# Kernel tuning notes

Measured on AMD Instinct MI355X. Metric: run time of the kernel, lower is better.

## Reference

```python
import jax, jax.numpy as jnp
import numpy as np

N, D, E = 32768, 768, 8
F = 4 * D  # 3072


def setup_inputs() -> dict:
    key = jax.random.key(0)
    ks = jax.random.split(key, 8)
    scale = 0.02
    hidden_states = jax.random.normal(ks[0], (N, D), dtype=jnp.float32)
    Wg = jax.random.normal(ks[1], (E, D), dtype=jnp.float32) * scale  # gate, no bias
    W1 = jax.random.normal(ks[2], (E, F, D), dtype=jnp.float32) * scale
    b1 = jnp.zeros((E, F), dtype=jnp.float32)
    W2 = jax.random.normal(ks[3], (E, D, F), dtype=jnp.float32) * scale
    b2 = jnp.zeros((E, D), dtype=jnp.float32)
    W3 = jax.random.normal(ks[4], (E, 1, D), dtype=jnp.float32) * scale
    b3 = jnp.zeros((E, 1), dtype=jnp.float32)
    return {"hidden_states": hidden_states, "Wg": Wg, "W1": W1, "b1": b1,
            "W2": W2, "b2": b2, "W3": W3, "b3": b3, "top_k": 2}


def reference(hidden_states, Wg, W1, b1, W2, b2, W3, b3, top_k):
    x = hidden_states  # [N, D]
    logits = x @ Wg.T  # [N, E]
    probs = jax.nn.softmax(logits.astype(jnp.float32), axis=-1)
    w, _sel = jax.lax.top_k(probs, top_k)  # [N, k] (descending)
    w = (w / w.sum(axis=-1, keepdims=True)).astype(x.dtype)
    # FAITHFUL TO SOURCE BUG: expert used is the position index j (experts[j]),
    # not the selected expert id. So densely run experts 0..top_k-1 on all tokens.
    W1k, b1k = W1[:top_k], b1[:top_k]
    W2k, b2k = W2[:top_k], b2[:top_k]
    W3k, b3k = W3[:top_k], b3[:top_k]
    # dropout is identity in eval mode
    h = jax.nn.relu(jnp.einsum('nd,kfd->knf', x, W1k) + b1k[:, None, :])  # [k,N,F]
    o = x[None, :, :] + jnp.einsum('knf,kdf->knd', h, W2k) + b2k[:, None, :]  # residual, [k,N,D]
    s = jnp.einsum('knd,kod->kno', o, W3k) + b3k[:, None, :]  # [k,N,1]
    out = jnp.sum(jnp.swapaxes(w, 0, 1)[:, :, None] * s, axis=0)  # [N,1]
    return out
```

## Files before the change

kernel.cpp:

```cpp
#include <hip/hip_runtime.h>
#include <hip/hip_bf16.h>
#include <stdint.h>

#define N_TOK 32768
#define DDIM  768
#define FDIM  3072
#define NCOLS (2*FDIM)
#define BK    32
#define KTILES (DDIM/BK)
#define NTILES (NCOLS/128)
#define VD_CHUNK 96

typedef __attribute__((ext_vector_type(8))) short bf16x8;
typedef __attribute__((ext_vector_type(4))) float f32x4;

__device__ __forceinline__ unsigned short f2bf(float f) {
  unsigned u = __builtin_bit_cast(unsigned, f);
  unsigned r = (u + 0x7fffu + ((u >> 16) & 1u)) >> 16;
  return (unsigned short)r;
}

__device__ __forceinline__ void gl_lds16(const void* g, void* l) {
  __builtin_amdgcn_global_load_lds(
      (const __attribute__((address_space(1))) unsigned int*)g,
      (__attribute__((address_space(3))) unsigned int*)l, 16, 0, 0);
}

__global__ __launch_bounds__(256) void cvt_kernel(const float* __restrict__ src,
                                                  unsigned short* __restrict__ dst) {
  size_t i = ((size_t)blockIdx.x * 256 + threadIdx.x) * 4;
  float4 f = *(const float4*)(src + i);
  ushort4 u;
  u.x = f2bf(f.x); u.y = f2bf(f.y); u.z = f2bf(f.z); u.w = f2bf(f.w);
  *(ushort4*)(dst + i) = u;
}

__global__ __launch_bounds__(256) void vcalc_kernel(const float* __restrict__ W2,
                                                    const float* __restrict__ W3,
                                                    float* __restrict__ vpart) {
  __shared__ float w3s[VD_CHUNK];
  int k  = blockIdx.x / 12;
  int fb = blockIdx.x % 12;
  int db = blockIdx.y;
  if (threadIdx.x < VD_CHUNK) w3s[threadIdx.x] = W3[k*DDIM + db*VD_CHUNK + threadIdx.x];
  __syncthreads();
  int f = fb*256 + threadIdx.x;
  const float* W2k = W2 + (size_t)k*DDIM*FDIM + (size_t)db*VD_CHUNK*FDIM + f;
  float s = 0.f;
  #pragma unroll 8
  for (int d = 0; d < VD_CHUNK; ++d) s += W2k[(size_t)d*FDIM] * w3s[d];
  vpart[(size_t)db*NCOLS + k*FDIM + f] = s;
}

__global__ __launch_bounds__(256) void vfinal_kernel(const float* __restrict__ vpart,
                                                     float* __restrict__ v,
                                                     const float* __restrict__ b2,
                                                     const float* __restrict__ W3,
                                                     const float* __restrict__ b3,
                                                     float* __restrict__ cbuf) {
  int f = blockIdx.x*256 + threadIdx.x;
  float s = 0.f;
  #pragma unroll
  for (int db = 0; db < 8; ++db) s += vpart[(size_t)db*NCOLS + f];
  v[f] = s;
  if (blockIdx.x == 0 && threadIdx.x < 128) {
    int k = threadIdx.x >> 6, lane = threadIdx.x & 63;
    float c = 0.f;
    #pragma unroll
    for (int it = 0; it < DDIM/64; ++it) {
      int i = it*64 + lane;
      c += b2[k*DDIM + i] * W3[k*DDIM + i];
    }
    #pragma unroll
    for (int m = 1; m < 64; m <<= 1) c += __shfl_xor(c, m, 64);
    if (lane == 0) cbuf[k] = c + b3[k];
  }
}

__global__ __launch_bounds__(256) void gate_cvt_kernel(
    const float* __restrict__ x, const float* __restrict__ Wg,
    const float* __restrict__ W3, const float* __restrict__ cbuf,
    unsigned short* __restrict__ xbf,
    float* __restrict__ wgt, float* __restrict__ base) {
  int wid  = threadIdx.x >> 6;
  int lane = threadIdx.x & 63;
  int n = blockIdx.x * 4 + wid;
  const float4* xr = (const float4*)(x + (size_t)n * DDIM);
  ushort4* xw = (ushort4*)(xbf + (size_t)n * DDIM);
  float acc[8] = {0,0,0,0,0,0,0,0};
  float d30 = 0.f, d31 = 0.f;
  #pragma unroll
  for (int it = 0; it < DDIM/256; ++it) {
    int i = it*64 + lane;
    float4 xv = xr[i];
    ushort4 u;
    u.x = f2bf(xv.x); u.y = f2bf(xv.y); u.z = f2bf(xv.z); u.w = f2bf(xv.w);
    xw[i] = u;
    #pragma unroll
    for (int e = 0; e < 8; ++e) {
      float4 w = ((const float4*)(Wg + e*DDIM))[i];
      acc[e] += xv.x*w.x + xv.y*w.y + xv.z*w.z + xv.w*w.w;
    }
    float4 wa = ((const float4*)W3)[i];
    d30 += xv.x*wa.x + xv.y*wa.y + xv.z*wa.z + xv.w*wa.w;
    float4 wb = ((const float4*)(W3 + DDIM))[i];
    d31 += xv.x*wb.x + xv.y*wb.y + xv.z*wb.z + xv.w*wb.w;
  }
  #pragma unroll
  for (int m = 1; m < 64; m <<= 1) {
    #pragma unroll
    for (int e = 0; e < 8; ++e) acc[e] += __shfl_xor(acc[e], m, 64);
    d30 += __shfl_xor(d30, m, 64);
    d31 += __shfl_xor(d31, m, 64);
  }
  if (lane == 0) {
    float l1 = acc[0]; int a1 = 0;
    #pragma unroll
    for (int e = 1; e < 8; ++e) if (acc[e] > l1) { l1 = acc[e]; a1 = e; }
    float l2 = -3.4e38f;
    #pragma unroll
    for (int e = 0; e < 8; ++e) if (e != a1 && acc[e] > l2) l2 = acc[e];
    float w0 = 1.f / (1.f + __expf(l2 - l1));
    float w1 = 1.f - w0;
    wgt[2*n]   = w0;
    wgt[2*n+1] = w1;
    base[n] = w0 * (d30 + cbuf[0]) + w1 * (d31 + cbuf[1]);
  }
}

__global__ __launch_bounds__(256) void gemm_kernel(
    const unsigned short* __restrict__ A,
    const unsigned short* __restrict__ B,
    const float* __restrict__ b1,
    const float* __restrict__ v,
    float* __restrict__ part) {
  __shared__ __align__(16) unsigned short As[128*BK];
  __shared__ __align__(16) unsigned short Bs[128*BK];
  __shared__ float red[256];

  const int tid  = threadIdx.x;
  const int lane = tid & 63, wid = tid >> 6;
  const int wr = wid >> 1, wc = wid & 1;
  const int q  = lane >> 4, cl = lane & 15;
  const int bn = blockIdx.x;
  const int bm = blockIdx.y;

  const int r0  = tid >> 2;
  const int kq0 = (tid & 3) ^ ((r0 >> 1) & 3);
  const int r1  = r0 + 64;
  const int kq1 = (tid & 3) ^ ((r1 >> 1) & 3);

  const unsigned short* Ab = A + (size_t)bm * 128 * DDIM;
  const unsigned short* Bb = B + (size_t)bn * 128 * DDIM;

  f32x4 zero = {0.f, 0.f, 0.f, 0.f};
  f32x4 acc[4][4];
  #pragma unroll
  for (int i = 0; i < 4; ++i)
    #pragma unroll
    for (int j = 0; j < 4; ++j) acc[i][j] = zero;

  int aoff[4], boff[4];
  #pragma unroll
  for (int i = 0; i < 4; ++i) {
    int ra = wr*64 + i*16 + cl;
    aoff[i] = (ra*4 + (q ^ ((ra>>1)&3))) * 16;
    int rb = wc*64 + i*16 + cl;
    boff[i] = (rb*4 + (q ^ ((rb>>1)&3))) * 16;
  }
  char* AsB = (char*)As;
  char* BsB = (char*)Bs;

  for (int kt = 0; kt < KTILES; ++kt) {
    int k0 = kt * BK;
    gl_lds16(Ab + (size_t)r0*DDIM + k0 + kq0*8, AsB + wid*1024);
    gl_lds16(Ab + (size_t)r1*DDIM + k0 + kq1*8, AsB + 4096 + wid*1024);
    gl_lds16(Bb + (size_t)r0*DDIM + k0 + kq0*8, BsB + wid*1024);
    gl_lds16(Bb + (size_t)r1*DDIM + k0 + kq1*8, BsB + 4096 + wid*1024);
    __syncthreads();
    bf16x8 af[4], bfr[4];
    #pragma unroll
    for (int i = 0; i < 4; ++i) {
      af[i]  = *(const bf16x8*)(AsB + aoff[i]);
      bfr[i] = *(const bf16x8*)(BsB + boff[i]);
    }
    #pragma unroll
    for (int i = 0; i < 4; ++i)
      #pragma unroll
      for (int j = 0; j < 4; ++j)
        acc[i][j] = __builtin_amdgcn_mfma_f32_16x16x32_bf16(af[i], bfr[j], acc[i][j], 0, 0, 0);
    __syncthreads();
  }

  float vv[4], bb[4];
  #pragma unroll
  for (int j = 0; j < 4; ++j) {
    int cg = bn*128 + wc*64 + j*16 + cl;
    vv[j] = v[cg];
    bb[j] = b1[cg];
  }
  #pragma unroll
  for (int i = 0; i < 4; ++i) {
    #pragma unroll
    for (int r = 0; r < 4; ++r) {
      float s = 0.f;
      #pragma unroll
      for (int j = 0; j < 4; ++j) {
        float val = acc[i][j][r] + bb[j];
        val = fmaxf(val, 0.f);
        s += val * vv[j];
      }
      #pragma unroll
      for (int m = 1; m < 16; m <<= 1) s += __shfl_xor(s, m, 64);
      if (cl == 0) red[(wr*64 + i*16 + q*4 + r)*2 + wc] = s;
    }
  }
  __syncthreads();
  if (tid < 128)
    part[(size_t)bn * N_TOK + bm*128 + tid] = red[tid*2] + red[tid*2+1];
}

__global__ __launch_bounds__(256) void final_kernel(const float* __restrict__ part,
                                                    const float* __restrict__ wgt,
                                                    const float* __restrict__ base,
                                                    float* __restrict__ out) {
  int n = blockIdx.x * 256 + threadIdx.x;
  float s0 = 0.f, s1 = 0.f;
  #pragma unroll
  for (int t = 0; t < 24; ++t) s0 += part[(size_t)t*N_TOK + n];
  #pragma unroll
  for (int t = 24; t < 48; ++t) s1 += part[(size_t)t*N_TOK + n];
  out[n] = base[n] + wgt[2*n]*s0 + wgt[2*n+1]*s1;
}

extern "C" void kernel_launch(void* const* d_in, const int* in_sizes, int n_in,
                              void* d_out, int out_size, void* d_ws, size_t ws_size,
                              hipStream_t stream) {
  const float* x  = (const float*)d_in[0];
  const float* Wg = (const float*)d_in[1];
  const float* W1 = (const float*)d_in[2];
  const float* b1 = (const float*)d_in[3];
  const float* W2 = (const float*)d_in[4];
  const float* b2 = (const float*)d_in[5];
  const float* W3 = (const float*)d_in[6];
  const float* b3 = (const float*)d_in[7];
  float* out = (float*)d_out;

  char* ws = (char*)d_ws;
  size_t off = 0;
  auto alloc = [&](size_t bytes) -> char* {
    char* p = ws + off;
    off += (bytes + 255) & ~(size_t)255;
    return p;
  };
  unsigned short* xbf  = (unsigned short*)alloc((size_t)N_TOK * DDIM * 2);
  unsigned short* w1bf = (unsigned short*)alloc((size_t)NCOLS * DDIM * 2);
  float* vpart = (float*)alloc((size_t)8 * NCOLS * 4);
  float* v     = (float*)alloc((size_t)NCOLS * 4);
  float* cbuf  = (float*)alloc(64);
  float* wgt   = (float*)alloc((size_t)N_TOK * 2 * 4);
  float* base  = (float*)alloc((size_t)N_TOK * 4);
  float* part  = (float*)alloc((size_t)NTILES * N_TOK * 4);
  if (off > ws_size) return;

  cvt_kernel<<<(NCOLS*DDIM)/1024, 256, 0, stream>>>(W1, w1bf);
  vcalc_kernel<<<dim3(24, 8), 256, 0, stream>>>(W2, W3, vpart);
  vfinal_kernel<<<NCOLS/256, 256, 0, stream>>>(vpart, v, b2, W3, b3, cbuf);
  gate_cvt_kernel<<<N_TOK/4, 256, 0, stream>>>(x, Wg, W3, cbuf, xbf, wgt, base);
  gemm_kernel<<<dim3(NTILES, N_TOK/128), 256, 0, stream>>>(xbf, w1bf, b1, v, part);
  final_kernel<<<N_TOK/256, 256, 0, stream>>>(part, wgt, base, out);
}
```

Measured before the change: 631.2 us.

## Warp-specialize GEMM with producer waves and a 4-stage LDS ring

```diff
diff --git a/kernel.cpp b/kernel.cpp
--- a/kernel.cpp
+++ b/kernel.cpp
@@ -10,6 +10,8 @@
 #define KTILES (DDIM/BK)
 #define NTILES (NCOLS/128)
 #define VD_CHUNK 96
+#define STAGES 4
+#define STAGE_BYTES 16384
 
 typedef __attribute__((ext_vector_type(8))) short bf16x8;
 typedef __attribute__((ext_vector_type(4))) float f32x4;
@@ -128,91 +130,114 @@
   }
 }
 
-__global__ __launch_bounds__(256) void gemm_kernel(
+__global__ __launch_bounds__(384) void gemm_kernel(
     const unsigned short* __restrict__ A,
     const unsigned short* __restrict__ B,
     const float* __restrict__ b1,
     const float* __restrict__ v,
     float* __restrict__ part) {
-  __shared__ __align__(16) unsigned short As[128*BK];
-  __shared__ __align__(16) unsigned short Bs[128*BK];
+  __shared__ __align__(16) char stg[STAGES * STAGE_BYTES];
   __shared__ float red[256];
+  __shared__ int flag[STAGES];
+  __shared__ int done[STAGES];
 
   const int tid  = threadIdx.x;
   const int lane = tid & 63, wid = tid >> 6;
-  const int wr = wid >> 1, wc = wid & 1;
-  const int q  = lane >> 4, cl = lane & 15;
   const int bn = blockIdx.x;
   const int bm = blockIdx.y;
 
-  const int r0  = tid >> 2;
-  const int kq0 = (tid & 3) ^ ((r0 >> 1) & 3);
-  const int r1  = r0 + 64;
-  const int kq1 = (tid & 3) ^ ((r1 >> 1) & 3);
+  if (tid < STAGES) { flag[tid] = 0; done[tid] = 0; }
+  __syncthreads();
 
   const unsigned short* Ab = A + (size_t)bm * 128 * DDIM;
   const unsigned short* Bb = B + (size_t)bn * 128 * DDIM;
 
-  f32x4 zero = {0.f, 0.f, 0.f, 0.f};
-  f32x4 acc[4][4];
-  #pragma unroll
-  for (int i = 0; i < 4; ++i)
-    #pragma unroll
-    for (int j = 0; j < 4; ++j) acc[i][j] = zero;
-
-  int aoff[4], boff[4];
-  #pragma unroll
-  for (int i = 0; i < 4; ++i) {
-    int ra = wr*64 + i*16 + cl;
-    aoff[i] = (ra*4 + (q ^ ((ra>>1)&3))) * 16;
-    int rb = wc*64 + i*16 + cl;
-    boff[i] = (rb*4 + (q ^ ((rb>>1)&3))) * 16;
-  }
-  char* AsB = (char*)As;
-  char* BsB = (char*)Bs;
-
-  for (int kt = 0; kt < KTILES; ++kt) {
-    int k0 = kt * BK;
-    gl_lds16(Ab + (size_t)r0*DDIM + k0 + kq0*8, AsB + wid*1024);
-    gl_lds16(Ab + (size_t)r1*DDIM + k0 + kq1*8, AsB + 4096 + wid*1024);
-    gl_lds16(Bb + (size_t)r0*DDIM + k0 + kq0*8, BsB + wid*1024);
-    gl_lds16(Bb + (size_t)r1*DDIM + k0 + kq1*8, BsB + 4096 + wid*1024);
-    __syncthreads();
-    bf16x8 af[4], bfr[4];
+  if (wid >= 4) {
+    const int p = wid - 4;
+    const int rbase = lane >> 2;
+    const int kqx   = lane & 3;
+    for (int kt = p; kt < KTILES; kt += 2) {
+      const int s = kt & (STAGES - 1);
+      const int u = kt >> 2;
+      while (__hip_atomic_load(&done[s], __ATOMIC_ACQUIRE, __HIP_MEMORY_SCOPE_WORKGROUP) < 4*u) {}
+      const int k0 = kt * BK;
+      char* sb = stg + s * STAGE_BYTES;
+      #pragma unroll
+      for (int t = 0; t < 8; ++t) {
+        int r  = t*16 + rbase;
+        int kq = kqx ^ ((r >> 1) & 3);
+        gl_lds16(Ab + (size_t)r*DDIM + k0 + kq*8, sb + t*1024);
+      }
+      #pragma unroll
+      for (int t = 0; t < 8; ++t) {
+        int r  = t*16 + rbase;
+        int kq = kqx ^ ((r >> 1) & 3);
+        gl_lds16(Bb + (size_t)r*DDIM + k0 + kq*8, sb + 8192 + t*1024);
+      }
+      __builtin_amdgcn_s_waitcnt(0x0F70);
+      __hip_atomic_store(&flag[s], kt + 1, __ATOMIC_RELEASE, __HIP_MEMORY_SCOPE_WORKGROUP);
+    }
+  } else {
+    const int wr = wid >> 1, wc = wid & 1;
+    const int q  = lane >> 4, cl = lane & 15;
+
+    f32x4 zero = {0.f, 0.f, 0.f, 0.f};
+    f32x4 acc[4][4];
+    #pragma unroll
+    for (int i = 0; i < 4; ++i)
+      #pragma unroll
+      for (int j = 0; j < 4; ++j) acc[i][j] = zero;
+
+    int aoff[4], boff[4];
     #pragma unroll
     for (int i = 0; i < 4; ++i) {
-      af[i]  = *(const bf16x8*)(AsB + aoff[i]);
-      bfr[i] = *(const bf16x8*)(BsB + boff[i]);
-    }
-    #pragma unroll
-    for (int i = 0; i < 4; ++i)
-      #pragma unroll
-      for (int j = 0; j < 4; ++j)
-        acc[i][j] = __builtin_amdgcn_mfma_f32_16x16x32_bf16(af[i], bfr[j], acc[i][j], 0, 0, 0);
-    __syncthreads();
-  }
-
-  float vv[4], bb[4];
-  #pragma unroll
-  for (int j = 0; j < 4; ++j) {
-    int cg = bn*128 + wc*64 + j*16 + cl;
-    vv[j] = v[cg];
-    bb[j] = b1[cg];
-  }
-  #pragma unroll
-  for (int i = 0; i < 4; ++i) {
-    #pragma unroll
-    for (int r = 0; r < 4; ++r) {
-      float s = 0.f;
-      #pragma unroll
-      for (int j = 0; j < 4; ++j) {
-        float val = acc[i][j][r] + bb[j];
-        val = fmaxf(val, 0.f);
-        s += val * vv[j];
-      }
-      #pragma unroll
-      for (int m = 1; m < 16; m <<= 1) s += __shfl_xor(s, m, 64);
-      if (cl == 0) red[(wr*64 + i*16 + q*4 + r)*2 + wc] = s;
+      int ra = wr*64 + i*16 + cl;
+      aoff[i] = (ra*4 + (q ^ ((ra >> 1) & 3))) * 16;
+      int rb = wc*64 + i*16 + cl;
+      boff[i] = (rb*4 + (q ^ ((rb >> 1) & 3))) * 16 + 8192;
+    }
+
+    for (int kt = 0; kt < KTILES; ++kt) {
+      const int s = kt & (STAGES - 1);
+      while (__hip_atomic_load(&flag[s], __ATOMIC_ACQUIRE, __HIP_MEMORY_SCOPE_WORKGROUP) < kt + 1) {}
+      const char* sb = stg + s * STAGE_BYTES;
+      bf16x8 af[4], bfr[4];
+      #pragma unroll
+      for (int i = 0; i < 4; ++i) {
+        af[i]  = *(const bf16x8*)(sb + aoff[i]);
+        bfr[i] = *(const bf16x8*)(sb + boff[i]);
+      }
+      if (lane == 0)
+        __hip_atomic_fetch_add(&done[s], 1, __ATOMIC_RELEASE, __HIP_MEMORY_SCOPE_WORKGROUP);
+      #pragma unroll
+      for (int i = 0; i < 4; ++i)
+        #pragma unroll
+        for (int j = 0; j < 4; ++j)
+          acc[i][j] = __builtin_amdgcn_mfma_f32_16x16x32_bf16(af[i], bfr[j], acc[i][j], 0, 0, 0);
+    }
+
+    float vv[4], bb[4];
+    #pragma unroll
+    for (int j = 0; j < 4; ++j) {
+      int cg = bn*128 + wc*64 + j*16 + cl;
+      vv[j] = v[cg];
+      bb[j] = b1[cg];
+    }
+    #pragma unroll
+    for (int i = 0; i < 4; ++i) {
+      #pragma unroll
+      for (int r = 0; r < 4; ++r) {
+        float s = 0.f;
+        #pragma unroll
+        for (int j = 0; j < 4; ++j) {
+          float val = acc[i][j][r] + bb[j];
+          val = fmaxf(val, 0.f);
+          s += val * vv[j];
+        }
+        #pragma unroll
+        for (int m = 1; m < 16; m <<= 1) s += __shfl_xor(s, m, 64);
+        if (cl == 0) red[(wr*64 + i*16 + q*4 + r)*2 + wc] = s;
+      }
     }
   }
   __syncthreads();
@@ -267,6 +292,6 @@
   vcalc_kernel<<<dim3(24, 8), 256, 0, stream>>>(W2, W3, vpart);
   vfinal_kernel<<<NCOLS/256, 256, 0, stream>>>(vpart, v, b2, W3, b3, cbuf);
   gate_cvt_kernel<<<N_TOK/4, 256, 0, stream>>>(x, Wg, W3, cbuf, xbf, wgt, base);
-  gemm_kernel<<<dim3(NTILES, N_TOK/128), 256, 0, stream>>>(xbf, w1bf, b1, v, part);
+  gemm_kernel<<<dim3(NTILES, N_TOK/128), 384, 0, stream>>>(xbf, w1bf, b1, v, part);
   final_kernel<<<N_TOK/256, 256, 0, stream>>>(part, wgt, base, out);
 }
```

After: 752.9 us. +19.3%, slower.

## Pre-tile bf16 operands and load MFMA fragments directly from global memory

Applied to the files above, without the earlier changes.

```diff
diff --git a/kernel.cpp b/kernel.cpp
--- a/kernel.cpp
+++ b/kernel.cpp
@@ -6,13 +6,13 @@
 #define DDIM  768
 #define FDIM  3072
 #define NCOLS (2*FDIM)
-#define BK    32
-#define KTILES (DDIM/BK)
-#define NTILES (NCOLS/128)
+#define KTILES 24
+#define NTILES 48
 #define VD_CHUNK 96
 
 typedef __attribute__((ext_vector_type(8))) short bf16x8;
 typedef __attribute__((ext_vector_type(4))) float f32x4;
+typedef __attribute__((ext_vector_type(8))) unsigned short u16x8;
 
 __device__ __forceinline__ unsigned short f2bf(float f) {
   unsigned u = __builtin_bit_cast(unsigned, f);
@@ -20,19 +20,20 @@
   return (unsigned short)r;
 }
 
-__device__ __forceinline__ void gl_lds16(const void* g, void* l) {
-  __builtin_amdgcn_global_load_lds(
-      (const __attribute__((address_space(1))) unsigned int*)g,
-      (__attribute__((address_space(3))) unsigned int*)l, 16, 0, 0);
-}
 
 __global__ __launch_bounds__(256) void cvt_kernel(const float* __restrict__ src,
                                                   unsigned short* __restrict__ dst) {
-  size_t i = ((size_t)blockIdx.x * 256 + threadIdx.x) * 4;
-  float4 f = *(const float4*)(src + i);
-  ushort4 u;
-  u.x = f2bf(f.x); u.y = f2bf(f.y); u.z = f2bf(f.z); u.w = f2bf(f.w);
-  *(ushort4*)(dst + i) = u;
+  int idx = blockIdx.x * 256 + threadIdx.x;
+  int g  = idx / 96;
+  int dg = idx % 96;
+  const float* s = src + (size_t)g * DDIM + dg * 8;
+  float4 f0 = *(const float4*)s;
+  float4 f1 = *(const float4*)(s + 4);
+  u16x8 u;
+  u[0]=f2bf(f0.x); u[1]=f2bf(f0.y); u[2]=f2bf(f0.z); u[3]=f2bf(f0.w);
+  u[4]=f2bf(f1.x); u[5]=f2bf(f1.y); u[6]=f2bf(f1.z); u[7]=f2bf(f1.w);
+  int bn = g >> 7, r = g & 127, kt = dg >> 2, qq = dg & 3;
+  *(u16x8*)(dst + ((size_t)(bn*24 + kt)*128 + r)*32 + qq*8) = u;
 }
 
 __global__ __launch_bounds__(256) void vcalc_kernel(const float* __restrict__ W2,
@@ -85,21 +86,22 @@
   int wid  = threadIdx.x >> 6;
   int lane = threadIdx.x & 63;
   int n = blockIdx.x * 4 + wid;
+  int bm = n >> 7, r = n & 127;
   const float4* xr = (const float4*)(x + (size_t)n * DDIM);
-  ushort4* xw = (ushort4*)(xbf + (size_t)n * DDIM);
   float acc[8] = {0,0,0,0,0,0,0,0};
   float d30 = 0.f, d31 = 0.f;
   #pragma unroll
-  for (int it = 0; it < DDIM/256; ++it) {
+  for (int it = 0; it < 3; ++it) {
     int i = it*64 + lane;
     float4 xv = xr[i];
     ushort4 u;
     u.x = f2bf(xv.x); u.y = f2bf(xv.y); u.z = f2bf(xv.z); u.w = f2bf(xv.w);
-    xw[i] = u;
-    #pragma unroll
-    for (int e = 0; e < 8; ++e) {
-      float4 w = ((const float4*)(Wg + e*DDIM))[i];
-      acc[e] += xv.x*w.x + xv.y*w.y + xv.z*w.z + xv.w*w.w;
+    int kt = i >> 3, qq = (i >> 1) & 3, e = (i & 1) * 4;
+    *(ushort4*)(xbf + ((size_t)(bm*24 + kt)*128 + r)*32 + qq*8 + e) = u;
+    #pragma unroll
+    for (int ee = 0; ee < 8; ++ee) {
+      float4 wv = ((const float4*)(Wg + ee*DDIM))[i];
+      acc[ee] += xv.x*wv.x + xv.y*wv.y + xv.z*wv.z + xv.w*wv.w;
     }
     float4 wa = ((const float4*)W3)[i];
     d30 += xv.x*wa.x + xv.y*wa.y + xv.z*wa.z + xv.w*wa.w;
@@ -128,30 +130,28 @@
   }
 }
 
-__global__ __launch_bounds__(256) void gemm_kernel(
+__global__ __launch_bounds__(256, 3) void gemm_kernel(
     const unsigned short* __restrict__ A,
     const unsigned short* __restrict__ B,
-    const float* __restrict__ b1,
+    const float* __restrict__ bias1,
     const float* __restrict__ v,
     float* __restrict__ part) {
-  __shared__ __align__(16) unsigned short As[128*BK];
-  __shared__ __align__(16) unsigned short Bs[128*BK];
   __shared__ float red[256];
-
   const int tid  = threadIdx.x;
   const int lane = tid & 63, wid = tid >> 6;
   const int wr = wid >> 1, wc = wid & 1;
   const int q  = lane >> 4, cl = lane & 15;
-  const int bn = blockIdx.x;
-  const int bm = blockIdx.y;
-
-  const int r0  = tid >> 2;
-  const int kq0 = (tid & 3) ^ ((r0 >> 1) & 3);
-  const int r1  = r0 + 64;
-  const int kq1 = (tid & 3) ^ ((r1 >> 1) & 3);
-
-  const unsigned short* Ab = A + (size_t)bm * 128 * DDIM;
-  const unsigned short* Bb = B + (size_t)bn * 128 * DDIM;
+
+  const int bidx = blockIdx.x;
+  const int xcd = bidx & 7, slot = bidx >> 3;
+  const int sup = slot / 48, w = slot % 48;
+  const int sg  = xcd * 32 + sup;
+  const int sm  = sg & 31, sn = sg >> 5;
+  const int bm  = sm * 8 + w / 6;
+  const int bn  = sn * 6 + w % 6;
+
+  const unsigned short* Ab = A + (size_t)bm * (KTILES*128*32) + (wr*64 + cl)*32 + q*8;
+  const unsigned short* Bb = B + (size_t)bn * (KTILES*128*32) + (wc*64 + cl)*32 + q*8;
 
   f32x4 zero = {0.f, 0.f, 0.f, 0.f};
   f32x4 acc[4][4];
@@ -160,36 +160,39 @@
     #pragma unroll
     for (int j = 0; j < 4; ++j) acc[i][j] = zero;
 
-  int aoff[4], boff[4];
+  bf16x8 af0[4], bf0[4], af1[4], bf1[4];
   #pragma unroll
   for (int i = 0; i < 4; ++i) {
-    int ra = wr*64 + i*16 + cl;
-    aoff[i] = (ra*4 + (q ^ ((ra>>1)&3))) * 16;
-    int rb = wc*64 + i*16 + cl;
-    boff[i] = (rb*4 + (q ^ ((rb>>1)&3))) * 16;
-  }
-  char* AsB = (char*)As;
-  char* BsB = (char*)Bs;
-
-  for (int kt = 0; kt < KTILES; ++kt) {
-    int k0 = kt * BK;
-    gl_lds16(Ab + (size_t)r0*DDIM + k0 + kq0*8, AsB + wid*1024);
-    gl_lds16(Ab + (size_t)r1*DDIM + k0 + kq1*8, AsB + 4096 + wid*1024);
-    gl_lds16(Bb + (size_t)r0*DDIM + k0 + kq0*8, BsB + wid*1024);
-    gl_lds16(Bb + (size_t)r1*DDIM + k0 + kq1*8, BsB + 4096 + wid*1024);
-    __syncthreads();
-    bf16x8 af[4], bfr[4];
+    af0[i] = *(const bf16x8*)(Ab + i*512);
+    bf0[i] = *(const bf16x8*)(Bb + i*512);
+  }
+  for (int kt = 0; kt < KTILES; kt += 2) {
+    const unsigned short* An = Ab + (size_t)(kt+1)*4096;
+    const unsigned short* Bn = Bb + (size_t)(kt+1)*4096;
     #pragma unroll
     for (int i = 0; i < 4; ++i) {
-      af[i]  = *(const bf16x8*)(AsB + aoff[i]);
-      bfr[i] = *(const bf16x8*)(BsB + boff[i]);
+      af1[i] = *(const bf16x8*)(An + i*512);
+      bf1[i] = *(const bf16x8*)(Bn + i*512);
     }
     #pragma unroll
     for (int i = 0; i < 4; ++i)
       #pragma unroll
       for (int j = 0; j < 4; ++j)
-        acc[i][j] = __builtin_amdgcn_mfma_f32_16x16x32_bf16(af[i], bfr[j], acc[i][j], 0, 0, 0);
-    __syncthreads();
+        acc[i][j] = __builtin_amdgcn_mfma_f32_16x16x32_bf16(af0[i], bf0[j], acc[i][j], 0, 0, 0);
+    if (kt + 2 < KTILES) {
+      const unsigned short* An2 = Ab + (size_t)(kt+2)*4096;
+      const unsigned short* Bn2 = Bb + (size_t)(kt+2)*4096;
+      #pragma unroll
+      for (int i = 0; i < 4; ++i) {
+        af0[i] = *(const bf16x8*)(An2 + i*512);
+        bf0[i] = *(const bf16x8*)(Bn2 + i*512);
+      }
+    }
+    #pragma unroll
+    for (int i = 0; i < 4; ++i)
+      #pragma unroll
+      for (int j = 0; j < 4; ++j)
+        acc[i][j] = __builtin_amdgcn_mfma_f32_16x16x32_bf16(af1[i], bf1[j], acc[i][j], 0, 0, 0);
   }
 
   float vv[4], bb[4];
@@ -197,7 +200,7 @@
   for (int j = 0; j < 4; ++j) {
     int cg = bn*128 + wc*64 + j*16 + cl;
     vv[j] = v[cg];
-    bb[j] = b1[cg];
+    bb[j] = bias1[cg];
   }
   #pragma unroll
   for (int i = 0; i < 4; ++i) {
@@ -263,10 +266,10 @@
   float* part  = (float*)alloc((size_t)NTILES * N_TOK * 4);
   if (off > ws_size) return;
 
-  cvt_kernel<<<(NCOLS*DDIM)/1024, 256, 0, stream>>>(W1, w1bf);
+  cvt_kernel<<<(NCOLS*96)/256, 256, 0, stream>>>(W1, w1bf);
   vcalc_kernel<<<dim3(24, 8), 256, 0, stream>>>(W2, W3, vpart);
   vfinal_kernel<<<NCOLS/256, 256, 0, stream>>>(vpart, v, b2, W3, b3, cbuf);
   gate_cvt_kernel<<<N_TOK/4, 256, 0, stream>>>(x, Wg, W3, cbuf, xbf, wgt, base);
-  gemm_kernel<<<dim3(NTILES, N_TOK/128), 256, 0, stream>>>(xbf, w1bf, b1, v, part);
+  gemm_kernel<<<NTILES*(N_TOK/128), 256, 0, stream>>>(xbf, w1bf, b1, v, part);
   final_kernel<<<N_TOK/256, 256, 0, stream>>>(part, wgt, base, out);
 }
```

Result: slower. 792.8 us (+25.6%).

## Double-buffer LDS tiles in GEMM to overlap global loads with MFMA

Applied to the files above, without the earlier changes.

```diff
diff --git a/kernel.cpp b/kernel.cpp
--- a/kernel.cpp
+++ b/kernel.cpp
@@ -134,8 +134,7 @@
     const float* __restrict__ b1,
     const float* __restrict__ v,
     float* __restrict__ part) {
-  __shared__ __align__(16) unsigned short As[128*BK];
-  __shared__ __align__(16) unsigned short Bs[128*BK];
+  __shared__ __align__(16) char stg[2 * 16384];
   __shared__ float red[256];
 
   const int tid  = threadIdx.x;
@@ -164,25 +163,35 @@
   #pragma unroll
   for (int i = 0; i < 4; ++i) {
     int ra = wr*64 + i*16 + cl;
-    aoff[i] = (ra*4 + (q ^ ((ra>>1)&3))) * 16;
+    aoff[i] = (ra*4 + (q ^ ((ra >> 1) & 3))) * 16;
     int rb = wc*64 + i*16 + cl;
-    boff[i] = (rb*4 + (q ^ ((rb>>1)&3))) * 16;
-  }
-  char* AsB = (char*)As;
-  char* BsB = (char*)Bs;
+    boff[i] = (rb*4 + (q ^ ((rb >> 1) & 3))) * 16 + 8192;
+  }
+
+  {
+    char* sb = stg;
+    gl_lds16(Ab + (size_t)r0*DDIM + kq0*8, sb + wid*1024);
+    gl_lds16(Ab + (size_t)r1*DDIM + kq1*8, sb + 4096 + wid*1024);
+    gl_lds16(Bb + (size_t)r0*DDIM + kq0*8, sb + 8192 + wid*1024);
+    gl_lds16(Bb + (size_t)r1*DDIM + kq1*8, sb + 12288 + wid*1024);
+  }
+  __syncthreads();
 
   for (int kt = 0; kt < KTILES; ++kt) {
-    int k0 = kt * BK;
-    gl_lds16(Ab + (size_t)r0*DDIM + k0 + kq0*8, AsB + wid*1024);
-    gl_lds16(Ab + (size_t)r1*DDIM + k0 + kq1*8, AsB + 4096 + wid*1024);
-    gl_lds16(Bb + (size_t)r0*DDIM + k0 + kq0*8, BsB + wid*1024);
-    gl_lds16(Bb + (size_t)r1*DDIM + k0 + kq1*8, BsB + 4096 + wid*1024);
-    __syncthreads();
+    if (kt + 1 < KTILES) {
+      const int k0 = (kt + 1) * BK;
+      char* sb = stg + ((kt + 1) & 1) * 16384;
+      gl_lds16(Ab + (size_t)r0*DDIM + k0 + kq0*8, sb + wid*1024);
+      gl_lds16(Ab + (size_t)r1*DDIM + k0 + kq1*8, sb + 4096 + wid*1024);
+      gl_lds16(Bb + (size_t)r0*DDIM + k0 + kq0*8, sb + 8192 + wid*1024);
+      gl_lds16(Bb + (size_t)r1*DDIM + k0 + kq1*8, sb + 12288 + wid*1024);
+    }
+    const char* cb = stg + (kt & 1) * 16384;
     bf16x8 af[4], bfr[4];
     #pragma unroll
     for (int i = 0; i < 4; ++i) {
-      af[i]  = *(const bf16x8*)(AsB + aoff[i]);
-      bfr[i] = *(const bf16x8*)(BsB + boff[i]);
+      af[i]  = *(const bf16x8*)(cb + aoff[i]);
+      bfr[i] = *(const bf16x8*)(cb + boff[i]);
     }
     #pragma unroll
     for (int i = 0; i < 4; ++i)
```

After: 680.5 us. +7.8%, slower.
